# Performance work log

Measured on AMD Instinct MI355X. Metric: run time of the kernel, lower is better.

Reference implementation:

```python
import jax, jax.numpy as jnp
import numpy as np

# ---- static config (mirrors MonitorRetina init) ----
N, S, H, W = 256, 1, 144, 256        # stimulus: [N, S, H, W]
HR, WR = 144, 256                    # retina height/width
FOV_HALF_RAD = 0.5 * 75.0 * np.pi / 180.0   # Angular retina, degrees=75
GELU_GAMMA = 1.7015043497085571      # variance-preserving gain for gelu
OUT_OF_RANGE = 10.0                  # grid value for rays missing the monitor


def isotropic_grid_2d(h, w):
    """Pixel-center coordinates, isotropic (normalized by max dim), [-1,1] on the long axis."""
    m = float(max(h, w))
    y = (jnp.arange(h, dtype=jnp.float32) * 2.0 + 1.0 - h) / m
    x = (jnp.arange(w, dtype=jnp.float32) * 2.0 + 1.0 - w) / m
    gy, gx = jnp.meshgrid(y, x, indexing="ij")
    return gx, gy  # each [h, w]


def rmat_3d(ax, ay, az):
    """Batched 3D rotation matrix R = Rz @ Ry @ Rx from Euler angles, each [N]."""
    cx, sx = jnp.cos(ax), jnp.sin(ax)
    cy, sy = jnp.cos(ay), jnp.sin(ay)
    cz, sz = jnp.cos(az), jnp.sin(az)
    one, zero = jnp.ones_like(ax), jnp.zeros_like(ax)
    Rx = jnp.stack([one, zero, zero, zero, cx, -sx, zero, sx, cx], -1).reshape(-1, 3, 3)
    Ry = jnp.stack([cy, zero, sy, zero, one, zero, -sy, zero, cy], -1).reshape(-1, 3, 3)
    Rz = jnp.stack([cz, -sz, zero, sz, cz, zero, zero, zero, one], -1).reshape(-1, 3, 3)
    return jnp.einsum("nij,njk,nkl->nil", Rz, Ry, Rx)  # [N,3,3]


def retina_rays(rmat):
    """Angular retina: pixel angles -> unit ray directions, rotated per batch. [N,HR,WR,3]."""
    gx, gy = isotropic_grid_2d(HR, WR)
    ax, ay = gx * FOV_HALF_RAD, gy * FOV_HALF_RAD
    a = jnp.sqrt(ax * ax + ay * ay) + 1e-12
    sinc = jnp.sin(a) / a
    d = jnp.stack([sinc * ax, sinc * ay, jnp.cos(a)], -1)  # [HR,WR,3]
    return jnp.einsum("nij,hwj->nhwi", rmat, d)


def monitor_project(rays):
    """Plane monitor at unit distance along +z: perspective divide to isotropic grid coords. [N,HR,WR,2]."""
    rz = rays[..., 2]
    safe = rz > 1e-3
    inv = jnp.where(safe, rz, 1.0)
    gx = jnp.where(safe, rays[..., 0] / inv, OUT_OF_RANGE)
    gy = jnp.where(safe, rays[..., 1] / inv, OUT_OF_RANGE)
    return jnp.stack([gx, gy], -1)


def isotropic_grid_sample_2d(x, grid, pad_value=0.0):
    """Bilinear sample x:[N,C,H,W] at grid:[N,H',W',2] (isotropic coords), constant padding."""
    m = float(max(H, W))
    px = (grid[..., 0] * m + W - 1.0) * 0.5  # [N,H',W'] pixel coords
    py = (grid[..., 1] * m + H - 1.0) * 0.5
    x0 = jnp.floor(px)
    y0 = jnp.floor(py)
    wx = px - x0
    wy = py - y0
    x0i = x0.astype(jnp.int32)
    y0i = y0.astype(jnp.int32)

    def corner(img, yi, xi):
        valid = (xi >= 0) & (xi < W) & (yi >= 0) & (yi < H)
        v = img[:, jnp.clip(yi, 0, H - 1), jnp.clip(xi, 0, W - 1)]  # [C,H',W']
        return jnp.where(valid[None], v, pad_value)

    def one(img, y0i, x0i, wx, wy):
        v00 = corner(img, y0i, x0i)
        v01 = corner(img, y0i, x0i + 1)
        v10 = corner(img, y0i + 1, x0i)
        v11 = corner(img, y0i + 1, x0i + 1)
        return (v00 * (1 - wx) + v01 * wx) * (1 - wy) + (v10 * (1 - wx) + v11 * wx) * wy

    return jax.vmap(one)(x, y0i, x0i, wx, wy)  # [N,C,H',W']


def setup_inputs() -> dict:
    key = jax.random.key(0)
    ks = jax.random.split(key, 8)
    F, D = 16, 128
    return {
        "stimulus": jax.random.normal(ks[0], (N, S, H, W), jnp.float32),
        "perspective": jax.random.normal(ks[1], (N, F), jnp.float32),
        "W1": jax.random.normal(ks[2], (F, D), jnp.float32) / np.sqrt(F),
        "b1": jnp.zeros((D,), jnp.float32),
        "W2": jax.random.normal(ks[3], (D, D), jnp.float32) / np.sqrt(D),
        "b2": jnp.zeros((D,), jnp.float32),
        "Wp": jax.random.normal(ks[4], (D, 3), jnp.float32) * 0.05,  # proj gains init near 0
        "bp": jnp.zeros((3,), jnp.float32),
    }


def reference(stimulus, perspective, W1, b1, W2, b2, Wp, bp):
    # MLP -> 3 angles -> rotation matrix (rmat)
    h = jax.nn.gelu(perspective @ W1 + b1) * GELU_GAMMA
    h = jax.nn.gelu(h @ W2 + b2) * GELU_GAMMA
    ang = h @ Wp + bp                      # [N,3]
    rm = rmat_3d(ang[:, 0], ang[:, 1], ang[:, 2])
    rays = retina_rays(rm)                 # [N,HR,WR,3]
    grid = monitor_project(rays)           # [N,HR,WR,2]
    # monitor_pixel / retina_pixel are Raw (identity) transforms
    return isotropic_grid_sample_2d(stimulus, grid, pad_value=0.0)  # [N,S,HR,WR]
```

## Files before the change

### kernel.cpp

```cpp
#include <hip/hip_runtime.h>
#include <math.h>

#define NB    256
#define IMG_H 144
#define IMG_W 256
#define IMG_ELEMS (IMG_H * IMG_W)
#define LDS_STRIDE 260
#define HR    144
#define WR    256
#define FDIM  16
#define DDIM  128

#define FOV_HALF_RAD 0.6544984694978736f
#define GELU_GAMMA   1.7015043497085571f
#define OUT_OF_RANGE 10.0f

typedef float f32x4 __attribute__((ext_vector_type(4)));

__device__ __forceinline__ float gelu_gamma(float x) {
    const float k0 = 0.7978845608028654f;
    const float k1 = 0.044715f;
    float t = tanhf(k0 * (x + k1 * x * x * x));
    return 0.5f * x * (1.0f + t) * GELU_GAMMA;
}

__global__ void __launch_bounds__(DDIM) mlp_rmat_kernel(
    const float* __restrict__ persp,
    const float* __restrict__ W1,
    const float* __restrict__ b1,
    const float* __restrict__ W2,
    const float* __restrict__ b2,
    const float* __restrict__ Wp,
    const float* __restrict__ bp,
    float* __restrict__ Rout)
{
    const int n = blockIdx.x;
    const int d = threadIdx.x;

    __shared__ float sh1[DDIM];
    __shared__ float sh2[DDIM];
    __shared__ float ang[3];

    float acc = b1[d];
#pragma unroll
    for (int f = 0; f < FDIM; ++f)
        acc += persp[n * FDIM + f] * W1[f * DDIM + d];
    sh1[d] = gelu_gamma(acc);
    __syncthreads();

    float acc2 = b2[d];
#pragma unroll 8
    for (int k = 0; k < DDIM; ++k)
        acc2 += sh1[k] * W2[k * DDIM + d];
    sh2[d] = gelu_gamma(acc2);
    __syncthreads();

    if (d < 3) {
        float a = bp[d];
#pragma unroll 8
        for (int k = 0; k < DDIM; ++k)
            a += sh2[k] * Wp[k * 3 + d];
        ang[d] = a;
    }
    __syncthreads();

    if (d == 0) {
        float cx = cosf(ang[0]), sx = sinf(ang[0]);
        float cy = cosf(ang[1]), sy = sinf(ang[1]);
        float cz = cosf(ang[2]), sz = sinf(ang[2]);
        float* R = Rout + n * 9;
        R[0] = cz * cy;  R[1] = cz * sy * sx - sz * cx;  R[2] = cz * sy * cx + sz * sx;
        R[3] = sz * cy;  R[4] = sz * sy * sx + cz * cx;  R[5] = sz * sy * cx - cz * sx;
        R[6] = -sy;      R[7] = cy * sx;                 R[8] = cy * cx;
    }
}

__global__ void __launch_bounds__(1024, 4) retina_sample_kernel(
    const float* __restrict__ stim,
    const float* __restrict__ Rmat,
    float* __restrict__ out)
{
    __shared__ float simg[IMG_H * LDS_STRIDE];

    const int tid = threadIdx.x;
    const int n   = blockIdx.x;

    const float* Rn = Rmat + n * 9;
    const float r0 = Rn[0], r1 = Rn[1], r2 = Rn[2];
    const float r3 = Rn[3], r4 = Rn[4], r5 = Rn[5];
    const float r6 = Rn[6], r7 = Rn[7], r8 = Rn[8];

    const float* __restrict__ img = stim + (size_t)n * IMG_ELEMS;

    {
        const f32x4* __restrict__ src = (const f32x4*)img;
#pragma unroll
        for (int p = 0; p < 9; ++p) {
            const int g   = tid + p * 1024;
            const int row = g >> 6;
            const int c4  = g & 63;
            *(f32x4*)&simg[row * LDS_STRIDE + c4 * 4] = src[g];
        }
    }
    __syncthreads();

#pragma unroll
    for (int p = 0; p < 9; ++p) {
        const int g   = tid + p * 1024;
        const int px0 = g * 4;
        const int h   = px0 >> 8;
        const int w0  = px0 & 255;

        const float gy  = (2.0f * h + 1.0f - 144.0f) * (1.0f / 256.0f);
        const float ayv = gy * FOV_HALF_RAD;
        const float ay2 = ayv * ayv;

        float wx_[4], wy_[4];
        int a00[4], a01[4], a10[4], a11[4];
        bool m00[4], m01[4], m10[4], m11[4];

#pragma unroll
        for (int j = 0; j < 4; ++j) {
            const float gx  = (2.0f * (w0 + j) + 1.0f - 256.0f) * (1.0f / 256.0f);
            const float axv = gx * FOV_HALF_RAD;
            const float t   = axv * axv + ay2;

            float sc = fmaf(t, 2.7557319e-6f, -1.9841270e-4f);
            sc = fmaf(t, sc,  8.3333333e-3f);
            sc = fmaf(t, sc, -1.6666667e-1f);
            sc = fmaf(t, sc,  1.0f);

            float ca = fmaf(t, 2.4801587e-5f, -1.3888889e-3f);
            ca = fmaf(t, ca,  4.1666667e-2f);
            ca = fmaf(t, ca, -0.5f);
            ca = fmaf(t, ca,  1.0f);

            const float dx = sc * axv, dy = sc * ayv, dz = ca;

            const float rx = r0 * dx + r1 * dy + r2 * dz;
            const float ry = r3 * dx + r4 * dy + r5 * dz;
            const float rz = r6 * dx + r7 * dy + r8 * dz;

            const float inv = __builtin_amdgcn_rcpf(rz);
            const bool safe = rz > 0.001f;
            const float gxp = safe ? rx * inv : OUT_OF_RANGE;
            const float gyp = safe ? ry * inv : OUT_OF_RANGE;

            const float px = fmaf(gxp, 256.0f, (float)(IMG_W - 1)) * 0.5f;
            const float py = fmaf(gyp, 256.0f, (float)(IMG_H - 1)) * 0.5f;

            const float x0f = floorf(px), y0f = floorf(py);
            wx_[j] = px - x0f;
            wy_[j] = py - y0f;
            const int x0 = (int)x0f, y0 = (int)y0f;
            const int x1 = x0 + 1,   y1 = y0 + 1;

            const int xc0 = min(max(x0, 0), IMG_W - 1);
            const int xc1 = min(max(x1, 0), IMG_W - 1);
            const int yc0 = min(max(y0, 0), IMG_H - 1);
            const int yc1 = min(max(y1, 0), IMG_H - 1);

            m00[j] = ((unsigned)x0 < IMG_W) & ((unsigned)y0 < IMG_H);
            m01[j] = ((unsigned)x1 < IMG_W) & ((unsigned)y0 < IMG_H);
            m10[j] = ((unsigned)x0 < IMG_W) & ((unsigned)y1 < IMG_H);
            m11[j] = ((unsigned)x1 < IMG_W) & ((unsigned)y1 < IMG_H);

            a00[j] = yc0 * LDS_STRIDE + xc0;
            a01[j] = yc0 * LDS_STRIDE + xc1;
            a10[j] = yc1 * LDS_STRIDE + xc0;
            a11[j] = yc1 * LDS_STRIDE + xc1;
        }

        float v00[4], v01[4], v10[4], v11[4];
#pragma unroll
        for (int j = 0; j < 4; ++j) {
            v00[j] = simg[a00[j]];
            v01[j] = simg[a01[j]];
            v10[j] = simg[a10[j]];
            v11[j] = simg[a11[j]];
        }

        f32x4 res;
#pragma unroll
        for (int j = 0; j < 4; ++j) {
            const float c00 = m00[j] ? v00[j] : 0.0f;
            const float c01 = m01[j] ? v01[j] : 0.0f;
            const float c10 = m10[j] ? v10[j] : 0.0f;
            const float c11 = m11[j] ? v11[j] : 0.0f;
            const float top = c00 * (1.0f - wx_[j]) + c01 * wx_[j];
            const float bot = c10 * (1.0f - wx_[j]) + c11 * wx_[j];
            res[j] = top * (1.0f - wy_[j]) + bot * wy_[j];
        }

        f32x4* dst = (f32x4*)(out + (size_t)n * IMG_ELEMS + px0);
        __builtin_nontemporal_store(res, dst);
    }
}

extern "C" void kernel_launch(void* const* d_in, const int* in_sizes, int n_in,
                              void* d_out, int out_size, void* d_ws, size_t ws_size,
                              hipStream_t stream) {
    const float* stimulus    = (const float*)d_in[0];
    const float* perspective = (const float*)d_in[1];
    const float* W1          = (const float*)d_in[2];
    const float* b1          = (const float*)d_in[3];
    const float* W2          = (const float*)d_in[4];
    const float* b2          = (const float*)d_in[5];
    const float* Wp          = (const float*)d_in[6];
    const float* bp          = (const float*)d_in[7];
    float* out = (float*)d_out;

    float* Rmat = (float*)d_ws;

    mlp_rmat_kernel<<<NB, DDIM, 0, stream>>>(
        perspective, W1, b1, W2, b2, Wp, bp, Rmat);

    retina_sample_kernel<<<NB, 1024, 0, stream>>>(stimulus, Rmat, out);
}
```

Measured before the change: 119.9 us.

## Fuse MLP into the sampling kernel and use a zero-padded LDS image

Merges the MLP/rotation kernel into the sampling kernel. Wave 0 computes the angles and rotation matrix while the other 15 waves load the image into LDS, which removes one launch and the global round trip for Rmat. The LDS image gets a zero border, so bilinear taps can skip the per-tap bounds masks and use clamped float coordinates. Each thread now produces one pixel per iteration instead of four, so the output stores are scalar rather than vector. The MLP now runs on a single wave of the sampling block, which adds serial latency before the sampling phase can start.

After: 115.6 us, median of 2. 1.04x faster.

```diff
diff --git a/kernel.cpp b/kernel.cpp
--- a/kernel.cpp
+++ b/kernel.cpp
@@ -5,11 +5,13 @@
 #define IMG_H 144
 #define IMG_W 256
 #define IMG_ELEMS (IMG_H * IMG_W)
-#define LDS_STRIDE 260
 #define HR    144
 #define WR    256
 #define FDIM  16
 #define DDIM  128
+
+#define STRIDE 260
+#define SIMG_FLOATS (147 * STRIDE + 4)
 
 #define FOV_HALF_RAD 0.6544984694978736f
 #define GELU_GAMMA   1.7015043497085571f
@@ -24,7 +26,8 @@
     return 0.5f * x * (1.0f + t) * GELU_GAMMA;
 }
 
-__global__ void __launch_bounds__(DDIM) mlp_rmat_kernel(
+__global__ void __launch_bounds__(1024, 4) fused_retina_kernel(
+    const float* __restrict__ stim,
     const float* __restrict__ persp,
     const float* __restrict__ W1,
     const float* __restrict__ b1,
@@ -32,168 +35,153 @@
     const float* __restrict__ b2,
     const float* __restrict__ Wp,
     const float* __restrict__ bp,
-    float* __restrict__ Rout)
+    float* __restrict__ out)
 {
-    const int n = blockIdx.x;
-    const int d = threadIdx.x;
-
+    __shared__ float simg[SIMG_FLOATS];
     __shared__ float sh1[DDIM];
     __shared__ float sh2[DDIM];
-    __shared__ float ang[3];
-
-    float acc = b1[d];
+    __shared__ float sAng[3];
+    __shared__ float sR[9];
+
+    const int tid  = threadIdx.x;
+    const int n    = blockIdx.x;
+    const int wid  = tid >> 6;
+    const int lane = tid & 63;
+
+    const float* __restrict__ img = stim + (size_t)n * IMG_ELEMS;
+
+    if (tid < 340) {
+        f32x4 z = {0.0f, 0.0f, 0.0f, 0.0f};
+        int idx;
+        if (tid < 195) {
+            const int rr = tid / 65;
+            const int g  = tid - rr * 65;
+            const int s  = (rr == 0) ? 0 : (144 + rr);
+            idx = s * STRIDE + g * 4;
+        } else if (tid < 339) {
+            idx = (tid - 194) * STRIDE;
+        } else {
+            idx = 147 * STRIDE;
+        }
+        *(f32x4*)&simg[idx] = z;
+    }
+
+    if (wid > 0) {
+        const int t = tid - 64;
+        const f32x4* __restrict__ src = (const f32x4*)img;
 #pragma unroll
-    for (int f = 0; f < FDIM; ++f)
-        acc += persp[n * FDIM + f] * W1[f * DDIM + d];
-    sh1[d] = gelu_gamma(acc);
-    __syncthreads();
-
-    float acc2 = b2[d];
+        for (int p = 0; p < 10; ++p) {
+            const int g = t + p * 960;
+            if (g < 9216) {
+                const int row = g >> 6;
+                const int c4  = g & 63;
+                *(f32x4*)&simg[(row + 1) * STRIDE + 4 + c4 * 4] = src[g];
+            }
+        }
+    } else {
+        float a0 = b1[lane], a1 = b1[lane + 64];
+#pragma unroll
+        for (int f = 0; f < FDIM; ++f) {
+            const float p = persp[n * FDIM + f];
+            a0 = fmaf(p, W1[f * DDIM + lane],      a0);
+            a1 = fmaf(p, W1[f * DDIM + lane + 64], a1);
+        }
+        sh1[lane]      = gelu_gamma(a0);
+        sh1[lane + 64] = gelu_gamma(a1);
+        asm volatile("s_waitcnt lgkmcnt(0)" ::: "memory");
+
+        float c0 = b2[lane], c1 = b2[lane + 64];
 #pragma unroll 8
-    for (int k = 0; k < DDIM; ++k)
-        acc2 += sh1[k] * W2[k * DDIM + d];
-    sh2[d] = gelu_gamma(acc2);
-    __syncthreads();
-
-    if (d < 3) {
-        float a = bp[d];
+        for (int k = 0; k < DDIM; ++k) {
+            const float s = sh1[k];
+            c0 = fmaf(s, W2[k * DDIM + lane],      c0);
+            c1 = fmaf(s, W2[k * DDIM + lane + 64], c1);
+        }
+        sh2[lane]      = gelu_gamma(c0);
+        sh2[lane + 64] = gelu_gamma(c1);
+        asm volatile("s_waitcnt lgkmcnt(0)" ::: "memory");
+
+        if (lane < 3) {
+            float a = bp[lane];
 #pragma unroll 8
-        for (int k = 0; k < DDIM; ++k)
-            a += sh2[k] * Wp[k * 3 + d];
-        ang[d] = a;
+            for (int k = 0; k < DDIM; ++k)
+                a = fmaf(sh2[k], Wp[k * 3 + lane], a);
+            sAng[lane] = a;
+        }
+        asm volatile("s_waitcnt lgkmcnt(0)" ::: "memory");
+
+        if (lane == 0) {
+            const float cx = cosf(sAng[0]), sx = sinf(sAng[0]);
+            const float cy = cosf(sAng[1]), sy = sinf(sAng[1]);
+            const float cz = cosf(sAng[2]), sz = sinf(sAng[2]);
+            sR[0] = cz * cy;  sR[1] = cz * sy * sx - sz * cx;  sR[2] = cz * sy * cx + sz * sx;
+            sR[3] = sz * cy;  sR[4] = sz * sy * sx + cz * cx;  sR[5] = sz * sy * cx - cz * sx;
+            sR[6] = -sy;      sR[7] = cy * sx;                 sR[8] = cy * cx;
+        }
     }
     __syncthreads();
 
-    if (d == 0) {
-        float cx = cosf(ang[0]), sx = sinf(ang[0]);
-        float cy = cosf(ang[1]), sy = sinf(ang[1]);
-        float cz = cosf(ang[2]), sz = sinf(ang[2]);
-        float* R = Rout + n * 9;
-        R[0] = cz * cy;  R[1] = cz * sy * sx - sz * cx;  R[2] = cz * sy * cx + sz * sx;
-        R[3] = sz * cy;  R[4] = sz * sy * sx + cz * cx;  R[5] = sz * sy * cx - cz * sx;
-        R[6] = -sy;      R[7] = cy * sx;                 R[8] = cy * cx;
-    }
-}
-
-__global__ void __launch_bounds__(1024, 4) retina_sample_kernel(
-    const float* __restrict__ stim,
-    const float* __restrict__ Rmat,
-    float* __restrict__ out)
-{
-    __shared__ float simg[IMG_H * LDS_STRIDE];
-
-    const int tid = threadIdx.x;
-    const int n   = blockIdx.x;
-
-    const float* Rn = Rmat + n * 9;
-    const float r0 = Rn[0], r1 = Rn[1], r2 = Rn[2];
-    const float r3 = Rn[3], r4 = Rn[4], r5 = Rn[5];
-    const float r6 = Rn[6], r7 = Rn[7], r8 = Rn[8];
-
-    const float* __restrict__ img = stim + (size_t)n * IMG_ELEMS;
-
-    {
-        const f32x4* __restrict__ src = (const f32x4*)img;
-#pragma unroll
-        for (int p = 0; p < 9; ++p) {
-            const int g   = tid + p * 1024;
-            const int row = g >> 6;
-            const int c4  = g & 63;
-            *(f32x4*)&simg[row * LDS_STRIDE + c4 * 4] = src[g];
-        }
-    }
-    __syncthreads();
-
-#pragma unroll
-    for (int p = 0; p < 9; ++p) {
-        const int g   = tid + p * 1024;
-        const int px0 = g * 4;
+    const float r0 = sR[0], r1 = sR[1], r2 = sR[2];
+    const float r3 = sR[3], r4 = sR[4], r5 = sR[5];
+    const float r6 = sR[6], r7 = sR[7], r8 = sR[8];
+
+    float* __restrict__ outn = out + (size_t)n * IMG_ELEMS;
+
+#pragma unroll 4
+    for (int it = 0; it < 36; ++it) {
+        const int px0 = it * 1024 + tid;
         const int h   = px0 >> 8;
-        const int w0  = px0 & 255;
-
-        const float gy  = (2.0f * h + 1.0f - 144.0f) * (1.0f / 256.0f);
+        const int w   = px0 & 255;
+
+        const float gx  = ((float)(2 * w + 1) - 256.0f) * (1.0f / 256.0f);
+        const float gy  = ((float)(2 * h + 1) - 144.0f) * (1.0f / 256.0f);
+        const float axv = gx * FOV_HALF_RAD;
         const float ayv = gy * FOV_HALF_RAD;
-        const float ay2 = ayv * ayv;
-
-        float wx_[4], wy_[4];
-        int a00[4], a01[4], a10[4], a11[4];
-        bool m00[4], m01[4], m10[4], m11[4];
-
-#pragma unroll
-        for (int j = 0; j < 4; ++j) {
-            const float gx  = (2.0f * (w0 + j) + 1.0f - 256.0f) * (1.0f / 256.0f);
-            const float axv = gx * FOV_HALF_RAD;
-            const float t   = axv * axv + ay2;
-
-            float sc = fmaf(t, 2.7557319e-6f, -1.9841270e-4f);
-            sc = fmaf(t, sc,  8.3333333e-3f);
-            sc = fmaf(t, sc, -1.6666667e-1f);
-            sc = fmaf(t, sc,  1.0f);
-
-            float ca = fmaf(t, 2.4801587e-5f, -1.3888889e-3f);
-            ca = fmaf(t, ca,  4.1666667e-2f);
-            ca = fmaf(t, ca, -0.5f);
-            ca = fmaf(t, ca,  1.0f);
-
-            const float dx = sc * axv, dy = sc * ayv, dz = ca;
-
-            const float rx = r0 * dx + r1 * dy + r2 * dz;
-            const float ry = r3 * dx + r4 * dy + r5 * dz;
-            const float rz = r6 * dx + r7 * dy + r8 * dz;
-
-            const float inv = __builtin_amdgcn_rcpf(rz);
-            const bool safe = rz > 0.001f;
-            const float gxp = safe ? rx * inv : OUT_OF_RANGE;
-            const float gyp = safe ? ry * inv : OUT_OF_RANGE;
-
-            const float px = fmaf(gxp, 256.0f, (float)(IMG_W - 1)) * 0.5f;
-            const float py = fmaf(gyp, 256.0f, (float)(IMG_H - 1)) * 0.5f;
-
-            const float x0f = floorf(px), y0f = floorf(py);
-            wx_[j] = px - x0f;
-            wy_[j] = py - y0f;
-            const int x0 = (int)x0f, y0 = (int)y0f;
-            const int x1 = x0 + 1,   y1 = y0 + 1;
-
-            const int xc0 = min(max(x0, 0), IMG_W - 1);
-            const int xc1 = min(max(x1, 0), IMG_W - 1);
-            const int yc0 = min(max(y0, 0), IMG_H - 1);
-            const int yc1 = min(max(y1, 0), IMG_H - 1);
-
-            m00[j] = ((unsigned)x0 < IMG_W) & ((unsigned)y0 < IMG_H);
-            m01[j] = ((unsigned)x1 < IMG_W) & ((unsigned)y0 < IMG_H);
-            m10[j] = ((unsigned)x0 < IMG_W) & ((unsigned)y1 < IMG_H);
-            m11[j] = ((unsigned)x1 < IMG_W) & ((unsigned)y1 < IMG_H);
-
-            a00[j] = yc0 * LDS_STRIDE + xc0;
-            a01[j] = yc0 * LDS_STRIDE + xc1;
-            a10[j] = yc1 * LDS_STRIDE + xc0;
-            a11[j] = yc1 * LDS_STRIDE + xc1;
-        }
-
-        float v00[4], v01[4], v10[4], v11[4];
-#pragma unroll
-        for (int j = 0; j < 4; ++j) {
-            v00[j] = simg[a00[j]];
-            v01[j] = simg[a01[j]];
-            v10[j] = simg[a10[j]];
-            v11[j] = simg[a11[j]];
-        }
-
-        f32x4 res;
-#pragma unroll
-        for (int j = 0; j < 4; ++j) {
-            const float c00 = m00[j] ? v00[j] : 0.0f;
-            const float c01 = m01[j] ? v01[j] : 0.0f;
-            const float c10 = m10[j] ? v10[j] : 0.0f;
-            const float c11 = m11[j] ? v11[j] : 0.0f;
-            const float top = c00 * (1.0f - wx_[j]) + c01 * wx_[j];
-            const float bot = c10 * (1.0f - wx_[j]) + c11 * wx_[j];
-            res[j] = top * (1.0f - wy_[j]) + bot * wy_[j];
-        }
-
-        f32x4* dst = (f32x4*)(out + (size_t)n * IMG_ELEMS + px0);
-        __builtin_nontemporal_store(res, dst);
+        const float tt  = fmaf(axv, axv, ayv * ayv);
+
+        float sc = fmaf(tt, 2.7557319e-6f, -1.9841270e-4f);
+        sc = fmaf(tt, sc,  8.3333333e-3f);
+        sc = fmaf(tt, sc, -1.6666667e-1f);
+        sc = fmaf(tt, sc,  1.0f);
+
+        float ca = fmaf(tt, 2.4801587e-5f, -1.3888889e-3f);
+        ca = fmaf(tt, ca,  4.1666667e-2f);
+        ca = fmaf(tt, ca, -0.5f);
+        ca = fmaf(tt, ca,  1.0f);
+
+        const float dx = sc * axv, dy = sc * ayv, dz = ca;
+
+        const float rx = fmaf(r0, dx, fmaf(r1, dy, r2 * dz));
+        const float ry = fmaf(r3, dx, fmaf(r4, dy, r5 * dz));
+        const float rz = fmaf(r6, dx, fmaf(r7, dy, r8 * dz));
+
+        const float inv  = __builtin_amdgcn_rcpf(rz);
+        const bool  safe = rz > 0.001f;
+        const float gxp  = safe ? rx * inv : OUT_OF_RANGE;
+        const float gyp  = safe ? ry * inv : OUT_OF_RANGE;
+
+        float pxf = fmaf(gxp, 256.0f, (float)(IMG_W - 1)) * 0.5f;
+        float pyf = fmaf(gyp, 256.0f, (float)(IMG_H - 1)) * 0.5f;
+        pxf = fminf(fmaxf(pxf, -1.0f), 256.0f);
+        pyf = fminf(fmaxf(pyf, -1.0f), 144.0f);
+
+        const float x0f = floorf(pxf), y0f = floorf(pyf);
+        const float wx  = pxf - x0f,   wy  = pyf - y0f;
+        const int   xi  = (int)x0f,    yi  = (int)y0f;
+
+        const int a00 = (yi + 1) * STRIDE + xi + 4;
+        const int a10 = a00 + STRIDE;
+
+        const float v00 = simg[a00];
+        const float v01 = simg[a00 + 1];
+        const float v10 = simg[a10];
+        const float v11 = simg[a10 + 1];
+
+        const float top = fmaf(wx, v01 - v00, v00);
+        const float bot = fmaf(wx, v11 - v10, v10);
+        const float res = fmaf(wy, bot - top, top);
+
+        __builtin_nontemporal_store(res, outn + px0);
     }
 }
 
@@ -210,10 +198,8 @@
     const float* bp          = (const float*)d_in[7];
     float* out = (float*)d_out;
 
-    float* Rmat = (float*)d_ws;
-
-    mlp_rmat_kernel<<<NB, DDIM, 0, stream>>>(
-        perspective, W1, b1, W2, b2, Wp, bp, Rmat);
-
-    retina_sample_kernel<<<NB, 1024, 0, stream>>>(stimulus, Rmat, out);
+    (void)d_ws; (void)ws_size;
+
+    fused_retina_kernel<<<NB, 1024, 0, stream>>>(
+        stimulus, perspective, W1, b1, W2, b2, Wp, bp, out);
 }
```

## Replace LDS-staged image with direct global gathers over many small blocks

Applied to the files above, without the earlier changes.

The sampling kernel no longer copies each whole 144x256 image into shared memory before gathering. Instead, 18 blocks of 256 threads per image each compute 8 rows and read the four bilinear taps straight from global memory, relying on L2 and the small per-image footprint. Block IDs are swizzled across groups of 8 so that blocks sharing an image may land together. This removes the full-image LDS staging and the large per-block shared-memory footprint that capped occupancy at one image per block, at the cost of possibly redundant, scattered global or cache reads and scalar stores instead of vector ones.

After: 130.9 us. 1.09x slower.

```diff
diff --git a/kernel.cpp b/kernel.cpp
--- a/kernel.cpp
+++ b/kernel.cpp
@@ -5,7 +5,6 @@
 #define IMG_H 144
 #define IMG_W 256
 #define IMG_ELEMS (IMG_H * IMG_W)
-#define LDS_STRIDE 260
 #define HR    144
 #define WR    256
 #define FDIM  16
@@ -14,6 +13,9 @@
 #define FOV_HALF_RAD 0.6544984694978736f
 #define GELU_GAMMA   1.7015043497085571f
 #define OUT_OF_RANGE 10.0f
+
+#define BLOCKS_PER_IMG 18
+#define K2_BLOCKS (NB * BLOCKS_PER_IMG)
 
 typedef float f32x4 __attribute__((ext_vector_type(4)));
 
@@ -44,14 +46,14 @@
     float acc = b1[d];
 #pragma unroll
     for (int f = 0; f < FDIM; ++f)
-        acc += persp[n * FDIM + f] * W1[f * DDIM + d];
+        acc = fmaf(persp[n * FDIM + f], W1[f * DDIM + d], acc);
     sh1[d] = gelu_gamma(acc);
     __syncthreads();
 
     float acc2 = b2[d];
 #pragma unroll 8
     for (int k = 0; k < DDIM; ++k)
-        acc2 += sh1[k] * W2[k * DDIM + d];
+        acc2 = fmaf(sh1[k], W2[k * DDIM + d], acc2);
     sh2[d] = gelu_gamma(acc2);
     __syncthreads();
 
@@ -59,7 +61,7 @@
         float a = bp[d];
 #pragma unroll 8
         for (int k = 0; k < DDIM; ++k)
-            a += sh2[k] * Wp[k * 3 + d];
+            a = fmaf(sh2[k], Wp[k * 3 + d], a);
         ang[d] = a;
     }
     __syncthreads();
@@ -75,125 +77,93 @@
     }
 }
 
-__global__ void __launch_bounds__(1024, 4) retina_sample_kernel(
+__global__ void __launch_bounds__(256, 4) retina_gather_kernel(
     const float* __restrict__ stim,
     const float* __restrict__ Rmat,
     float* __restrict__ out)
 {
-    __shared__ float simg[IMG_H * LDS_STRIDE];
+    const int per = K2_BLOCKS / 8;
+    const int bid = blockIdx.x;
+    const int wg  = (bid & 7) * per + (bid >> 3);
 
-    const int tid = threadIdx.x;
-    const int n   = blockIdx.x;
+    const int n   = wg / BLOCKS_PER_IMG;
+    const int blk = wg - n * BLOCKS_PER_IMG;
+    const int h0  = blk * 8;
+    const int w   = threadIdx.x;
 
-    const float* Rn = Rmat + n * 9;
+    const float* __restrict__ Rn = Rmat + n * 9;
     const float r0 = Rn[0], r1 = Rn[1], r2 = Rn[2];
     const float r3 = Rn[3], r4 = Rn[4], r5 = Rn[5];
     const float r6 = Rn[6], r7 = Rn[7], r8 = Rn[8];
 
-    const float* __restrict__ img = stim + (size_t)n * IMG_ELEMS;
+    const float* __restrict__ img  = stim + (size_t)n * IMG_ELEMS;
+    float* __restrict__ outn = out + (size_t)n * IMG_ELEMS + (size_t)h0 * IMG_W;
 
-    {
-        const f32x4* __restrict__ src = (const f32x4*)img;
-#pragma unroll
-        for (int p = 0; p < 9; ++p) {
-            const int g   = tid + p * 1024;
-            const int row = g >> 6;
-            const int c4  = g & 63;
-            *(f32x4*)&simg[row * LDS_STRIDE + c4 * 4] = src[g];
-        }
-    }
-    __syncthreads();
+    const float gx  = ((float)(2 * w + 1) - 256.0f) * (1.0f / 256.0f);
+    const float axv = gx * FOV_HALF_RAD;
+    const float ax2 = axv * axv;
 
-#pragma unroll
-    for (int p = 0; p < 9; ++p) {
-        const int g   = tid + p * 1024;
-        const int px0 = g * 4;
-        const int h   = px0 >> 8;
-        const int w0  = px0 & 255;
+#pragma unroll 4
+    for (int i = 0; i < 8; ++i) {
+        const int h = h0 + i;
+        const float gy  = ((float)(2 * h + 1) - 144.0f) * (1.0f / 256.0f);
+        const float ayv = gy * FOV_HALF_RAD;
+        const float tt  = fmaf(ayv, ayv, ax2);
 
-        const float gy  = (2.0f * h + 1.0f - 144.0f) * (1.0f / 256.0f);
-        const float ayv = gy * FOV_HALF_RAD;
-        const float ay2 = ayv * ayv;
+        float sc = fmaf(tt, 2.7557319e-6f, -1.9841270e-4f);
+        sc = fmaf(tt, sc,  8.3333333e-3f);
+        sc = fmaf(tt, sc, -1.6666667e-1f);
+        sc = fmaf(tt, sc,  1.0f);
 
-        float wx_[4], wy_[4];
-        int a00[4], a01[4], a10[4], a11[4];
-        bool m00[4], m01[4], m10[4], m11[4];
+        float ca = fmaf(tt, 2.4801587e-5f, -1.3888889e-3f);
+        ca = fmaf(tt, ca,  4.1666667e-2f);
+        ca = fmaf(tt, ca, -0.5f);
+        ca = fmaf(tt, ca,  1.0f);
 
-#pragma unroll
-        for (int j = 0; j < 4; ++j) {
-            const float gx  = (2.0f * (w0 + j) + 1.0f - 256.0f) * (1.0f / 256.0f);
-            const float axv = gx * FOV_HALF_RAD;
-            const float t   = axv * axv + ay2;
+        const float dx = sc * axv, dy = sc * ayv, dz = ca;
 
-            float sc = fmaf(t, 2.7557319e-6f, -1.9841270e-4f);
-            sc = fmaf(t, sc,  8.3333333e-3f);
-            sc = fmaf(t, sc, -1.6666667e-1f);
-            sc = fmaf(t, sc,  1.0f);
+        const float rx = fmaf(r0, dx, fmaf(r1, dy, r2 * dz));
+        const float ry = fmaf(r3, dx, fmaf(r4, dy, r5 * dz));
+        const float rz = fmaf(r6, dx, fmaf(r7, dy, r8 * dz));
 
-            float ca = fmaf(t, 2.4801587e-5f, -1.3888889e-3f);
-            ca = fmaf(t, ca,  4.1666667e-2f);
-            ca = fmaf(t, ca, -0.5f);
-            ca = fmaf(t, ca,  1.0f);
+        const float inv  = __builtin_amdgcn_rcpf(rz);
+        const bool  safe = rz > 0.001f;
+        const float gxp  = safe ? rx * inv : OUT_OF_RANGE;
+        const float gyp  = safe ? ry * inv : OUT_OF_RANGE;
 
-            const float dx = sc * axv, dy = sc * ayv, dz = ca;
+        const float pxf = fmaf(gxp, 256.0f, (float)(IMG_W - 1)) * 0.5f;
+        const float pyf = fmaf(gyp, 256.0f, (float)(IMG_H - 1)) * 0.5f;
 
-            const float rx = r0 * dx + r1 * dy + r2 * dz;
-            const float ry = r3 * dx + r4 * dy + r5 * dz;
-            const float rz = r6 * dx + r7 * dy + r8 * dz;
+        const float x0f = floorf(pxf), y0f = floorf(pyf);
+        const float wx  = pxf - x0f,   wy  = pyf - y0f;
+        const int   x0  = (int)x0f,    y0  = (int)y0f;
+        const int   x1  = x0 + 1,      y1  = y0 + 1;
 
-            const float inv = __builtin_amdgcn_rcpf(rz);
-            const bool safe = rz > 0.001f;
-            const float gxp = safe ? rx * inv : OUT_OF_RANGE;
-            const float gyp = safe ? ry * inv : OUT_OF_RANGE;
+        const bool vx0 = (unsigned)x0 < IMG_W;
+        const bool vx1 = (unsigned)x1 < IMG_W;
+        const bool vy0 = (unsigned)y0 < IMG_H;
+        const bool vy1 = (unsigned)y1 < IMG_H;
 
-            const float px = fmaf(gxp, 256.0f, (float)(IMG_W - 1)) * 0.5f;
-            const float py = fmaf(gyp, 256.0f, (float)(IMG_H - 1)) * 0.5f;
+        const int xc0 = min(max(x0, 0), IMG_W - 1);
+        const int xc1 = min(max(x1, 0), IMG_W - 1);
+        const int yb0 = min(max(y0, 0), IMG_H - 1) << 8;
+        const int yb1 = min(max(y1, 0), IMG_H - 1) << 8;
 
-            const float x0f = floorf(px), y0f = floorf(py);
-            wx_[j] = px - x0f;
-            wy_[j] = py - y0f;
-            const int x0 = (int)x0f, y0 = (int)y0f;
-            const int x1 = x0 + 1,   y1 = y0 + 1;
+        const float l00 = img[yb0 + xc0];
+        const float l01 = img[yb0 + xc1];
+        const float l10 = img[yb1 + xc0];
+        const float l11 = img[yb1 + xc1];
 
-            const int xc0 = min(max(x0, 0), IMG_W - 1);
-            const int xc1 = min(max(x1, 0), IMG_W - 1);
-            const int yc0 = min(max(y0, 0), IMG_H - 1);
-            const int yc1 = min(max(y1, 0), IMG_H - 1);
+        const float c00 = (vx0 & vy0) ? l00 : 0.0f;
+        const float c01 = (vx1 & vy0) ? l01 : 0.0f;
+        const float c10 = (vx0 & vy1) ? l10 : 0.0f;
+        const float c11 = (vx1 & vy1) ? l11 : 0.0f;
 
-            m00[j] = ((unsigned)x0 < IMG_W) & ((unsigned)y0 < IMG_H);
-            m01[j] = ((unsigned)x1 < IMG_W) & ((unsigned)y0 < IMG_H);
-            m10[j] = ((unsigned)x0 < IMG_W) & ((unsigned)y1 < IMG_H);
-            m11[j] = ((unsigned)x1 < IMG_W) & ((unsigned)y1 < IMG_H);
+        const float top = fmaf(wx, c01 - c00, c00);
+        const float bot = fmaf(wx, c11 - c10, c10);
+        const float res = fmaf(wy, bot - top, top);
 
-            a00[j] = yc0 * LDS_STRIDE + xc0;
-            a01[j] = yc0 * LDS_STRIDE + xc1;
-            a10[j] = yc1 * LDS_STRIDE + xc0;
-            a11[j] = yc1 * LDS_STRIDE + xc1;
-        }
-
-        float v00[4], v01[4], v10[4], v11[4];
-#pragma unroll
-        for (int j = 0; j < 4; ++j) {
-            v00[j] = simg[a00[j]];
-            v01[j] = simg[a01[j]];
-            v10[j] = simg[a10[j]];
-            v11[j] = simg[a11[j]];
-        }
-
-        f32x4 res;
-#pragma unroll
-        for (int j = 0; j < 4; ++j) {
-            const float c00 = m00[j] ? v00[j] : 0.0f;
-            const float c01 = m01[j] ? v01[j] : 0.0f;
-            const float c10 = m10[j] ? v10[j] : 0.0f;
-            const float c11 = m11[j] ? v11[j] : 0.0f;
-            const float top = c00 * (1.0f - wx_[j]) + c01 * wx_[j];
-            const float bot = c10 * (1.0f - wx_[j]) + c11 * wx_[j];
-            res[j] = top * (1.0f - wy_[j]) + bot * wy_[j];
-        }
-
-        f32x4* dst = (f32x4*)(out + (size_t)n * IMG_ELEMS + px0);
-        __builtin_nontemporal_store(res, dst);
+        __builtin_nontemporal_store(res, outn + i * IMG_W + w);
     }
 }
 
@@ -215,5 +185,5 @@
     mlp_rmat_kernel<<<NB, DDIM, 0, stream>>>(
         perspective, W1, b1, W2, b2, Wp, bp, Rmat);
 
-    retina_sample_kernel<<<NB, 1024, 0, stream>>>(stimulus, Rmat, out);
+    retina_gather_kernel<<<K2_BLOCKS, 256, 0, stream>>>(stimulus, Rmat, out);
 }
```
